# Kernel tuning notes

Measured on AMD Instinct MI355X. Metric: run time of the kernel, lower is better.

Reference implementation:

```python
import jax, jax.numpy as jnp
import numpy as np

NUM_HEADS = 16

def setup_inputs() -> dict:
    key = jax.random.key(0)
    k1, k2, k3 = jax.random.split(key, 3)
    B, N, C = 2, 2048, 1024
    x = jax.random.normal(k1, (B, N, C), dtype=jnp.float32)
    Wqkv = jax.random.normal(k2, (3 * C, C), dtype=jnp.float32) * (C ** -0.5)
    Wproj = jax.random.normal(k3, (C, C), dtype=jnp.float32) * (C ** -0.5)
    bproj = jnp.zeros((C,), dtype=jnp.float32)
    return {"x": x, "Wqkv": Wqkv, "Wproj": Wproj, "bproj": bproj}

def reference(x, Wqkv, Wproj, bproj):
    B, N, C = x.shape
    H = NUM_HEADS
    D = C // H
    scale = D ** -0.5
    # torch Linear: y = x @ W^T ; qkv -> [B,N,3,H,D]
    qkv = (x @ Wqkv.T).reshape(B, N, 3, H, D)
    q = qkv[:, :, 0].transpose(0, 2, 1, 3)  # [B,H,N,D]
    k = qkv[:, :, 1].transpose(0, 2, 1, 3)
    v = qkv[:, :, 2].transpose(0, 2, 1, 3)
    attn = jnp.einsum('bhnd,bhmd->bhnm', q, k) * scale  # [B,H,N,N]
    attn = jax.nn.softmax(attn, axis=-1)
    out = jnp.einsum('bhnm,bhmd->bhnd', attn, v)  # [B,H,N,D]
    out = out.transpose(0, 2, 1, 3).reshape(B, N, C)
    return out @ Wproj.T + bproj
```

## Files before the change

### kernel.cpp

```cpp
#include <hip/hip_runtime.h>

typedef unsigned short u16;
typedef unsigned int u32;
typedef __attribute__((ext_vector_type(8))) short short8;
typedef __attribute__((ext_vector_type(8))) __bf16 bf16x8;
typedef __attribute__((ext_vector_type(4))) float f32x4;
typedef __attribute__((ext_vector_type(16))) float f32x16;
typedef __attribute__((ext_vector_type(4))) unsigned short us4;
typedef __attribute__((ext_vector_type(4))) unsigned int u32x4;

#define DEVFN static __device__ __forceinline__

DEVFN u16 f2bf(float f) {
  u32 u = __float_as_uint(f);
  return (u16)((u + 0x7fffu + ((u >> 16) & 1u)) >> 16);
}

#if __has_builtin(__builtin_amdgcn_exp2f)
DEVFN float fexp2(float x) { return __builtin_amdgcn_exp2f(x); }
#else
DEVFN float fexp2(float x) { return exp2f(x); }
#endif

template <typename T>
DEVFN auto mfma16_imp(T a, T b, f32x4 c, int)
    -> decltype(__builtin_amdgcn_mfma_f32_16x16x32_bf16(a, b, c, 0, 0, 0)) {
  return __builtin_amdgcn_mfma_f32_16x16x32_bf16(a, b, c, 0, 0, 0);
}
template <typename T>
DEVFN f32x4 mfma16_imp(T a, T b, f32x4 c, long) {
  return __builtin_amdgcn_mfma_f32_16x16x32_bf16(
      __builtin_bit_cast(bf16x8, a), __builtin_bit_cast(bf16x8, b), c, 0, 0, 0);
}
DEVFN f32x4 MFMA(short8 a, short8 b, f32x4 c) { return mfma16_imp(a, b, c, 0); }

template <typename T>
DEVFN auto mfma32_imp(T a, T b, f32x16 c, int)
    -> decltype(__builtin_amdgcn_mfma_f32_32x32x16_bf16(a, b, c, 0, 0, 0)) {
  return __builtin_amdgcn_mfma_f32_32x32x16_bf16(a, b, c, 0, 0, 0);
}
template <typename T>
DEVFN f32x16 mfma32_imp(T a, T b, f32x16 c, long) {
  return __builtin_amdgcn_mfma_f32_32x32x16_bf16(
      __builtin_bit_cast(bf16x8, a), __builtin_bit_cast(bf16x8, b), c, 0, 0, 0);
}
DEVFN f32x16 MFMA32(short8 a, short8 b, f32x16 c) { return mfma32_imp(a, b, c, 0); }

DEVFN void gload_lds16(const u16* g, u16* l) {
  __builtin_amdgcn_global_load_lds(
      (__attribute__((address_space(1))) void*)g,
      (__attribute__((address_space(3))) void*)l, 16, 0, 0);
}

DEVFN u32 cvtpk_bf16(float lo, float hi) {
  u32 w;
  asm("v_cvt_pk_bf16_f32 %0, %1, %2" : "=v"(w) : "v"(lo), "v"(hi));
  return w;
}

__global__ void __launch_bounds__(256) cvt_kernel(const float* __restrict__ in,
                                                  u16* __restrict__ out, int n4) {
  int i = blockIdx.x * 256 + threadIdx.x;
  if (i < n4) {
    f32x4 v = ((const f32x4*)in)[i];
    us4 o;
    o[0] = f2bf(v[0]); o[1] = f2bf(v[1]); o[2] = f2bf(v[2]); o[3] = f2bf(v[3]);
    ((us4*)out)[i] = o;
  }
}

template <int F32OUT>
__global__ void __launch_bounds__(256) gemm_bt(
    const u16* __restrict__ A, const u16* __restrict__ Bm,
    u16* __restrict__ Cbf, float* __restrict__ Cf, const float* __restrict__ bias,
    int M, int N, int K) {
  __shared__ u16 As[128 * 32];
  __shared__ u16 Bs[128 * 32];
  const int tid = threadIdx.x;
  const int wave = tid >> 6, lane = tid & 63;
  const int bm = blockIdx.x * 128, bn = blockIdx.y * 128;
  const int wr = (wave >> 1) * 64, wc = (wave & 1) * 64;
  const int srow = lane >> 2, scol = (lane & 3) * 8;
  const int fr = lane & 15, fk = (lane >> 4) * 8;

  f32x4 acc[4][4] = {};

  for (int k0 = 0; k0 < K; k0 += 32) {
    __syncthreads();
#pragma unroll
    for (int t = 0; t < 2; ++t) {
      int rr = (wave * 2 + t) * 16 + srow;
      gload_lds16(A + (size_t)(bm + rr) * K + k0 + scol, As + (wave * 2 + t) * 512);
      gload_lds16(Bm + (size_t)(bn + rr) * K + k0 + scol, Bs + (wave * 2 + t) * 512);
    }
    __syncthreads();
    short8 af[4], bf[4];
#pragma unroll
    for (int i = 0; i < 4; ++i) {
      af[i] = *(const short8*)(As + (wr + i * 16 + fr) * 32 + fk);
      bf[i] = *(const short8*)(Bs + (wc + i * 16 + fr) * 32 + fk);
    }
#pragma unroll
    for (int mi = 0; mi < 4; ++mi)
#pragma unroll
      for (int ni = 0; ni < 4; ++ni)
        acc[mi][ni] = MFMA(af[mi], bf[ni], acc[mi][ni]);
  }

  const int orow = (lane >> 4) * 4, ocol = lane & 15;
#pragma unroll
  for (int mi = 0; mi < 4; ++mi)
#pragma unroll
    for (int ni = 0; ni < 4; ++ni)
#pragma unroll
      for (int r = 0; r < 4; ++r) {
        size_t row = (size_t)(bm + wr + mi * 16 + orow + r);
        size_t col = (size_t)(bn + wc + ni * 16 + ocol);
        if (F32OUT)
          Cf[row * N + col] = acc[mi][ni][r] + bias[col];
        else
          Cbf[row * N + col] = f2bf(acc[mi][ni][r]);
      }
}

__global__ void __launch_bounds__(256) attn_kernel(const u16* __restrict__ qkv,
                                                   u16* __restrict__ attn_out) {
  __shared__ u16 Ks[64 * 64];
  __shared__ u16 Vs[64 * 64];

  const int tid = threadIdx.x;
  const int wave = tid >> 6, lane = tid & 63;
  const int q5 = lane & 31, hi = lane >> 5;
  const int qb = blockIdx.x, h = blockIdx.y, b = blockIdx.z;
  const size_t tok0 = (size_t)b * 2048;
  const float SCALE = 0.18033688011112042f;

  const size_t qrow = tok0 + qb * 128 + wave * 32 + q5;
  const u16* qp = qkv + qrow * 3072 + h * 64 + hi * 8;
  short8 qf[4];
#pragma unroll
  for (int ks = 0; ks < 4; ++ks) qf[ks] = *(const short8*)(qp + ks * 16);

  const u16* kbase = qkv + tok0 * 3072 + 1024 + h * 64;
  const u16* vbase = qkv + tok0 * 3072 + 2048 + h * 64;

  const int k_srcoff = (((lane & 7) ^ (lane >> 3)) * 8);
  const int k_rowl = lane >> 3;

  float m_run = -1e30f, l_run = 0.f;
  f32x16 o0 = {}, o1 = {};

  for (int kv0 = 0; kv0 < 2048; kv0 += 64) {
    __syncthreads();
#pragma unroll
    for (int c = 0; c < 2; ++c) {
      int row = (c * 4 + wave) * 8 + k_rowl;
      gload_lds16(kbase + (size_t)(kv0 + row) * 3072 + k_srcoff,
                  Ks + (c * 4 + wave) * 512);
    }
#pragma unroll
    for (int c = 0; c < 2; ++c) {
      int gg = c * 256 + tid;
      int kv = gg >> 3, d0 = (gg & 7) * 8;
      short8 vv = *(const short8*)(vbase + (size_t)(kv0 + kv) * 3072 + d0);
      int kvhi = kv >> 3, kvlo = kv & 7;
#pragma unroll
      for (int i = 0; i < 8; ++i) {
        int d = d0 + i;
        Vs[d * 64 + ((kvhi ^ (d & 7) ^ ((d >> 3) & 7)) * 8) + kvlo] = (u16)vv[i];
      }
    }
    __syncthreads();

    f32x16 s0 = {}, s1 = {};
#pragma unroll
    for (int ks = 0; ks < 4; ++ks) {
      int ch = ((ks * 2 + hi) ^ (q5 & 7)) * 8;
      short8 k0 = *(const short8*)(Ks + q5 * 64 + ch);
      short8 k1 = *(const short8*)(Ks + (32 + q5) * 64 + ch);
      s0 = MFMA32(k0, qf[ks], s0);
      s1 = MFMA32(k1, qf[ks], s1);
    }

    float pmax = s0[0];
#pragma unroll
    for (int i = 1; i < 16; ++i) pmax = fmaxf(pmax, s0[i]);
#pragma unroll
    for (int i = 0; i < 16; ++i) pmax = fmaxf(pmax, s1[i]);
    pmax = fmaxf(pmax, __shfl_xor(pmax, 32, 64));
    float mraw = pmax * SCALE;

    if (__any(mraw > m_run + 8.f)) {
      float mn = fmaxf(m_run, mraw);
      float alpha = fexp2(m_run - mn);
#pragma unroll
      for (int i = 0; i < 16; ++i) { o0[i] *= alpha; o1[i] *= alpha; }
      l_run *= alpha;
      m_run = mn;
    }

    float p0[16], p1[16];
    float rs = 0.f;
#pragma unroll
    for (int i = 0; i < 16; ++i) {
      p0[i] = fexp2(fmaf(s0[i], SCALE, -m_run));
      p1[i] = fexp2(fmaf(s1[i], SCALE, -m_run));
      rs += p0[i] + p1[i];
    }
    rs += __shfl_xor(rs, 32, 64);
    l_run += rs;

    u32 w0[4][2], w1[4][2];
#pragma unroll
    for (int a = 0; a < 4; ++a) {
      w0[a][0] = cvtpk_bf16(p0[4 * a], p0[4 * a + 1]);
      w0[a][1] = cvtpk_bf16(p0[4 * a + 2], p0[4 * a + 3]);
      w1[a][0] = cvtpk_bf16(p1[4 * a], p1[4 * a + 1]);
      w1[a][1] = cvtpk_bf16(p1[4 * a + 2], p1[4 * a + 3]);
    }
    short8 pb[4];
#pragma unroll
    for (int ks = 0; ks < 4; ++ks) {
      int e = ks & 1;
      u32 x0 = (ks < 2) ? w0[2 * e][0] : w1[2 * e][0];
      u32 y0 = (ks < 2) ? w0[2 * e + 1][0] : w1[2 * e + 1][0];
      u32 x1 = (ks < 2) ? w0[2 * e][1] : w1[2 * e][1];
      u32 y1 = (ks < 2) ? w0[2 * e + 1][1] : w1[2 * e + 1][1];
      asm("v_permlane32_swap_b32 %0, %1" : "+v"(x0), "+v"(y0));
      asm("v_permlane32_swap_b32 %0, %1" : "+v"(x1), "+v"(y1));
      u32x4 t = {x0, x1, y0, y1};
      pb[ks] = __builtin_bit_cast(short8, t);
    }

#pragma unroll
    for (int ks = 0; ks < 4; ++ks) {
      int ch0 = ((ks * 2 + hi) ^ (q5 & 7) ^ ((q5 >> 3) & 7)) * 8;
      int ch1 = ch0 ^ (4 * 8);
      short8 v0 = *(const short8*)(Vs + q5 * 64 + ch0);
      short8 v1 = *(const short8*)(Vs + (32 + q5) * 64 + ch1);
      o0 = MFMA32(v0, pb[ks], o0);
      o1 = MFMA32(v1, pb[ks], o1);
    }
  }

  float inv = 1.f / l_run;
#pragma unroll
  for (int dt = 0; dt < 2; ++dt)
#pragma unroll
    for (int g = 0; g < 4; ++g) {
      us4 st;
#pragma unroll
      for (int c2 = 0; c2 < 4; ++c2) {
        float val = (dt == 0 ? o0[4 * g + c2] : o1[4 * g + c2]) * inv;
        st[c2] = f2bf(val);
      }
      int col = h * 64 + dt * 32 + 8 * g + 4 * hi;
      *(us4*)(attn_out + qrow * 1024 + col) = st;
    }
}

extern "C" void kernel_launch(void* const* d_in, const int* in_sizes, int n_in,
                              void* d_out, int out_size, void* d_ws, size_t ws_size,
                              hipStream_t stream) {
  const float* x = (const float*)d_in[0];
  const float* Wqkv = (const float*)d_in[1];
  const float* Wproj = (const float*)d_in[2];
  const float* bproj = (const float*)d_in[3];
  float* out = (float*)d_out;

  char* ws = (char*)d_ws;
  u16* x_bf     = (u16*)(ws);
  u16* wqkv_bf  = (u16*)(ws + 8388608);
  u16* wproj_bf = (u16*)(ws + 14680064);
  u16* qkv_bf   = (u16*)(ws + 16777216);
  u16* attn_bf  = (u16*)(ws + 41943040);

  cvt_kernel<<<4096, 256, 0, stream>>>(x, x_bf, 1048576);
  cvt_kernel<<<3072, 256, 0, stream>>>(Wqkv, wqkv_bf, 786432);
  cvt_kernel<<<1024, 256, 0, stream>>>(Wproj, wproj_bf, 262144);

  dim3 g1(32, 24);
  gemm_bt<0><<<g1, 256, 0, stream>>>(x_bf, wqkv_bf, qkv_bf, nullptr, nullptr,
                                     4096, 3072, 1024);

  dim3 g2(16, 16, 2);
  attn_kernel<<<g2, 256, 0, stream>>>(qkv_bf, attn_bf);

  dim3 g3(32, 8);
  gemm_bt<1><<<g3, 256, 0, stream>>>(attn_bf, wproj_bf, nullptr, out, bproj,
                                     4096, 1024, 1024);
}
```

Measured before the change: 137.8 us.

## Double-buffer K/V tiles in attention to overlap loads with compute

Splits the attention kernel's K and V shared-memory tiles into two buffers. The next tile's K is loaded straight into LDS and its V is held in registers while the current tile's QK and PV MFMAs run. V is scattered into the other buffer only after compute, which cuts the loop to one barrier per iteration. The row-max reduction also becomes a tree to shorten its dependency chain. This doubles LDS use and adds register pressure from the prefetched V values, which may lower occupancy.

```diff
diff --git a/kernel.cpp b/kernel.cpp
--- a/kernel.cpp
+++ b/kernel.cpp
@@ -56,6 +56,21 @@
   u32 w;
   asm("v_cvt_pk_bf16_f32 %0, %1, %2" : "=v"(w) : "v"(lo), "v"(hi));
   return w;
+}
+
+DEVFN void vscatter(int tid, short8 a, short8 b, u16* dst) {
+#pragma unroll
+  for (int c = 0; c < 2; ++c) {
+    short8 vv = c ? b : a;
+    int gg = c * 256 + tid;
+    int kv = gg >> 3, d0 = (gg & 7) * 8;
+    int kvhi = kv >> 3, kvlo = kv & 7;
+#pragma unroll
+    for (int i = 0; i < 8; ++i) {
+      int d = d0 + i;
+      dst[d * 64 + ((kvhi ^ (d & 7) ^ ((d >> 3) & 7)) * 8) + kvlo] = (u16)vv[i];
+    }
+  }
 }
 
 __global__ void __launch_bounds__(256) cvt_kernel(const float* __restrict__ in,
@@ -125,8 +140,8 @@
 
 __global__ void __launch_bounds__(256) attn_kernel(const u16* __restrict__ qkv,
                                                    u16* __restrict__ attn_out) {
-  __shared__ u16 Ks[64 * 64];
-  __shared__ u16 Vs[64 * 64];
+  __shared__ u16 Ks[2][64 * 64];
+  __shared__ u16 Vs[2][64 * 64];
 
   const int tid = threadIdx.x;
   const int wave = tid >> 6, lane = tid & 63;
@@ -146,47 +161,56 @@
 
   const int k_srcoff = (((lane & 7) ^ (lane >> 3)) * 8);
   const int k_rowl = lane >> 3;
+  const int v_kv0 = tid >> 3, v_d0 = (tid & 7) * 8;
+  const int v_kv1 = (256 + tid) >> 3;
 
   float m_run = -1e30f, l_run = 0.f;
   f32x16 o0 = {}, o1 = {};
 
-  for (int kv0 = 0; kv0 < 2048; kv0 += 64) {
-    __syncthreads();
-#pragma unroll
-    for (int c = 0; c < 2; ++c) {
-      int row = (c * 4 + wave) * 8 + k_rowl;
-      gload_lds16(kbase + (size_t)(kv0 + row) * 3072 + k_srcoff,
-                  Ks + (c * 4 + wave) * 512);
-    }
-#pragma unroll
-    for (int c = 0; c < 2; ++c) {
-      int gg = c * 256 + tid;
-      int kv = gg >> 3, d0 = (gg & 7) * 8;
-      short8 vv = *(const short8*)(vbase + (size_t)(kv0 + kv) * 3072 + d0);
-      int kvhi = kv >> 3, kvlo = kv & 7;
-#pragma unroll
-      for (int i = 0; i < 8; ++i) {
-        int d = d0 + i;
-        Vs[d * 64 + ((kvhi ^ (d & 7) ^ ((d >> 3) & 7)) * 8) + kvlo] = (u16)vv[i];
+#pragma unroll
+  for (int c = 0; c < 2; ++c) {
+    int row = (c * 4 + wave) * 8 + k_rowl;
+    gload_lds16(kbase + (size_t)row * 3072 + k_srcoff, Ks[0] + (c * 4 + wave) * 512);
+  }
+  {
+    short8 va = *(const short8*)(vbase + (size_t)v_kv0 * 3072 + v_d0);
+    short8 vb = *(const short8*)(vbase + (size_t)v_kv1 * 3072 + v_d0);
+    vscatter(tid, va, vb, Vs[0]);
+  }
+  __syncthreads();
+
+  for (int t = 0; t < 32; ++t) {
+    const int cur = t & 1, nxt = cur ^ 1;
+    const int kv1 = (t + 1) << 6;
+    short8 vna = {}, vnb = {};
+    if (t < 31) {
+#pragma unroll
+      for (int c = 0; c < 2; ++c) {
+        int row = (c * 4 + wave) * 8 + k_rowl;
+        gload_lds16(kbase + (size_t)(kv1 + row) * 3072 + k_srcoff,
+                    Ks[nxt] + (c * 4 + wave) * 512);
       }
-    }
-    __syncthreads();
-
+      vna = *(const short8*)(vbase + (size_t)(kv1 + v_kv0) * 3072 + v_d0);
+      vnb = *(const short8*)(vbase + (size_t)(kv1 + v_kv1) * 3072 + v_d0);
+    }
+
+    const u16* Kc = Ks[cur];
     f32x16 s0 = {}, s1 = {};
 #pragma unroll
     for (int ks = 0; ks < 4; ++ks) {
       int ch = ((ks * 2 + hi) ^ (q5 & 7)) * 8;
-      short8 k0 = *(const short8*)(Ks + q5 * 64 + ch);
-      short8 k1 = *(const short8*)(Ks + (32 + q5) * 64 + ch);
+      short8 k0 = *(const short8*)(Kc + q5 * 64 + ch);
+      short8 k1 = *(const short8*)(Kc + (32 + q5) * 64 + ch);
       s0 = MFMA32(k0, qf[ks], s0);
       s1 = MFMA32(k1, qf[ks], s1);
     }
 
-    float pmax = s0[0];
-#pragma unroll
-    for (int i = 1; i < 16; ++i) pmax = fmaxf(pmax, s0[i]);
-#pragma unroll
-    for (int i = 0; i < 16; ++i) pmax = fmaxf(pmax, s1[i]);
+    float mt[8];
+#pragma unroll
+    for (int i = 0; i < 8; ++i)
+      mt[i] = fmaxf(fmaxf(s0[i], s0[i + 8]), fmaxf(s1[i], s1[i + 8]));
+    float pmax = fmaxf(fmaxf(fmaxf(mt[0], mt[1]), fmaxf(mt[2], mt[3])),
+                       fmaxf(fmaxf(mt[4], mt[5]), fmaxf(mt[6], mt[7])));
     pmax = fmaxf(pmax, __shfl_xor(pmax, 32, 64));
     float mraw = pmax * SCALE;
 
@@ -228,19 +252,24 @@
       u32 y1 = (ks < 2) ? w0[2 * e + 1][1] : w1[2 * e + 1][1];
       asm("v_permlane32_swap_b32 %0, %1" : "+v"(x0), "+v"(y0));
       asm("v_permlane32_swap_b32 %0, %1" : "+v"(x1), "+v"(y1));
-      u32x4 t = {x0, x1, y0, y1};
-      pb[ks] = __builtin_bit_cast(short8, t);
-    }
-
+      u32x4 tt = {x0, x1, y0, y1};
+      pb[ks] = __builtin_bit_cast(short8, tt);
+    }
+
+    const u16* Vc = Vs[cur];
 #pragma unroll
     for (int ks = 0; ks < 4; ++ks) {
       int ch0 = ((ks * 2 + hi) ^ (q5 & 7) ^ ((q5 >> 3) & 7)) * 8;
       int ch1 = ch0 ^ (4 * 8);
-      short8 v0 = *(const short8*)(Vs + q5 * 64 + ch0);
-      short8 v1 = *(const short8*)(Vs + (32 + q5) * 64 + ch1);
+      short8 v0 = *(const short8*)(Vc + q5 * 64 + ch0);
+      short8 v1 = *(const short8*)(Vc + (32 + q5) * 64 + ch1);
       o0 = MFMA32(v0, pb[ks], o0);
       o1 = MFMA32(v1, pb[ks], o1);
     }
+
+    if (t < 31) vscatter(tid, vna, vnb, Vs[nxt]);
+
+    __syncthreads();
   }
 
   float inv = 1.f / l_run;
```

Result: no change. 140.4 us (+1.9%).
